# Performance work log

Measured on AMD Instinct MI355X. Metric: run time of the kernel, lower is better.

Reference implementation:

```python
import jax, jax.numpy as jnp
import numpy as np

N, D, H, O, E = 4096, 1024, 4096, 1024, 8
TOP_K = 2

def setup_inputs() -> dict:
    key = jax.random.key(0)
    k = jax.random.split(key, 4)
    x  = jax.random.normal(k[0], (N, D), dtype=jnp.float32)
    Wg = jax.random.normal(k[1], (D, E), dtype=jnp.float32) * (1.0 / np.sqrt(D))
    W1 = jax.random.normal(k[2], (E, D, H), dtype=jnp.float32) * (1.0 / np.sqrt(D))
    b1 = jnp.zeros((E, H), dtype=jnp.float32)
    W2 = jax.random.normal(k[3], (E, H, O), dtype=jnp.float32) * (1.0 / np.sqrt(H))
    b2 = jnp.zeros((E, O), dtype=jnp.float32)
    return {"x": x, "Wg": Wg, "W1": W1, "b1": b1, "W2": W2, "b2": b2}

def reference(x, Wg, W1, b1, W2, b2):
    # Gate: Linear(bias=False) -> ReLU (lin() appends act) -> softmax
    logits = jax.nn.relu(x @ Wg)                      # [N, E]
    probs = jax.nn.softmax(logits, axis=1)            # [N, E]
    top_p, sel = jax.lax.top_k(probs, TOP_K)          # [N, K]
    top_p = top_p / jnp.sum(top_p, axis=-1, keepdims=True)
    # Per-token combine weights over experts: [N, E]
    combine = jnp.sum(jax.nn.one_hot(sel, E, dtype=x.dtype) * top_p[..., None], axis=1)
    # Experts: ReLU(x W1 + b1) -> ReLU(h W2 + b2); final ReLU because lin() adds act on output layer
    h = jax.nn.relu(jnp.einsum('nd,edh->enh', x, W1) + b1[:, None, :])   # [E, N, H]
    y = jax.nn.relu(jnp.einsum('enh,eho->eno', h, W2) + b2[:, None, :])  # [E, N, O]
    out = jnp.einsum('eno,ne->no', y, combine)                            # [N, O]
    return out
```

## Files before the change

### kernel.cpp

```cpp
#include <hip/hip_runtime.h>
#include <cstdint>

#define NTOK 4096
#define DDIM 1024
#define HDIM 4096
#define ODIM 1024
#define NEXP 8
#define NSLOT (2*NTOK)
#define MAXT128 72
#define MAXT256 40

typedef __bf16 bf16x8 __attribute__((ext_vector_type(8)));
typedef float  f32x4  __attribute__((ext_vector_type(4)));
typedef unsigned short ushort8v __attribute__((ext_vector_type(8)));

__device__ __forceinline__ unsigned short f2bf(float f) {
    union { float f; unsigned int u; } v; v.f = f;
    unsigned int r = (v.u + 0x7FFF + ((v.u >> 16) & 1)) >> 16;
    return (unsigned short)r;
}

typedef const void __attribute__((address_space(1)))* gas_ptr;
typedef void       __attribute__((address_space(3)))* las_ptr;

__global__ void gate_kernel(const float* __restrict__ x, const float* __restrict__ Wg,
                            int2* __restrict__ sel, float2* __restrict__ wts,
                            int* __restrict__ counts, unsigned short* __restrict__ xb) {
    int wave = threadIdx.x >> 6;
    int lane = threadIdx.x & 63;
    int n = blockIdx.x * 4 + wave;
    float acc[NEXP];
#pragma unroll
    for (int e = 0; e < NEXP; e++) acc[e] = 0.f;
    const float* xr = x + (size_t)n * DDIM;
    unsigned short* xbr = xb + (size_t)n * DDIM;
#pragma unroll
    for (int i = 0; i < 4; i++) {
        int d = i * 256 + lane * 4;
        float4 xv = *(const float4*)&xr[d];
        ushort4 o;
        o.x = f2bf(xv.x); o.y = f2bf(xv.y); o.z = f2bf(xv.z); o.w = f2bf(xv.w);
        *(ushort4*)&xbr[d] = o;
        const float* wr = Wg + (size_t)d * NEXP;
#pragma unroll
        for (int jj = 0; jj < 4; jj++) {
            float xs = (jj == 0) ? xv.x : (jj == 1) ? xv.y : (jj == 2) ? xv.z : xv.w;
#pragma unroll
            for (int e = 0; e < NEXP; e++)
                acc[e] = fmaf(xs, wr[jj * NEXP + e], acc[e]);
        }
    }
#pragma unroll
    for (int e = 0; e < NEXP; e++) {
#pragma unroll
        for (int off = 32; off >= 1; off >>= 1)
            acc[e] += __shfl_xor(acc[e], off, 64);
    }
    if (lane == 0) {
        float l0 = -1e30f, l1 = -1e30f; int e0 = 0, e1 = 0;
#pragma unroll
        for (int e = 0; e < NEXP; e++) {
            float v = fmaxf(acc[e], 0.f);
            if (v > l0)      { l1 = l0; e1 = e0; l0 = v; e0 = e; }
            else if (v > l1) { l1 = v;  e1 = e; }
        }
        float w0 = 1.f / (1.f + expf(l1 - l0));
        sel[n] = make_int2(e0, e1);
        wts[n] = make_float2(w0, 1.f - w0);
        atomicAdd(&counts[e0], 1);
        atomicAdd(&counts[e1], 1);
    }
}

__global__ void route_kernel(const int2* __restrict__ sel, const float2* __restrict__ wts,
                             const int* __restrict__ counts, int* __restrict__ offsets,
                             int4* __restrict__ t128, int* __restrict__ nt128,
                             int4* __restrict__ t256, int* __restrict__ nt256,
                             int* __restrict__ slot_token, float* __restrict__ slot_weight) {
    __shared__ int cur[NEXP];
    int t = threadIdx.x;
    if (t == 0) {
        int s = 0, n1 = 0, n2 = 0;
        for (int e = 0; e < NEXP; e++) {
            offsets[e] = s; cur[e] = s;
            int c = counts[e];
            for (int r = 0; r < c; r += 128)
                t128[n1++] = make_int4(e, s + r, min(128, c - r), 0);
            for (int r = 0; r < c; r += 256)
                t256[n2++] = make_int4(e, s + r, min(256, c - r), 0);
            s += c;
        }
        offsets[NEXP] = s;
        *nt128 = n1; *nt256 = n2;
    }
    __syncthreads();
    for (int n = t; n < NTOK; n += blockDim.x) {
        int2 se = sel[n]; float2 w = wts[n];
        int p0 = atomicAdd(&cur[se.x], 1);
        slot_token[p0] = n; slot_weight[p0] = w.x;
        int p1 = atomicAdd(&cur[se.y], 1);
        slot_token[p1] = n; slot_weight[p1] = w.y;
    }
}

__global__ void transpose_cast_kernel(const float* __restrict__ src, unsigned short* __restrict__ dst,
                                      int R, int C) {
    __shared__ float tile[64][65];
    int e = blockIdx.z;
    const float* s = src + (size_t)e * R * C;
    unsigned short* d = dst + (size_t)e * R * C;
    int t = threadIdx.x;
    int r0 = blockIdx.y * 64, c0 = blockIdx.x * 64;
#pragma unroll
    for (int p = 0; p < 4; p++) {
        int r = p * 16 + (t >> 4);
        int c = (t & 15) * 4;
        float4 v = *(const float4*)&s[(size_t)(r0 + r) * C + (c0 + c)];
        tile[r][c] = v.x; tile[r][c + 1] = v.y; tile[r][c + 2] = v.z; tile[r][c + 3] = v.w;
    }
    __syncthreads();
    int c = t >> 2, rb = (t & 3) * 16;
#pragma unroll
    for (int j = 0; j < 2; j++) {
        ushort8v v;
#pragma unroll
        for (int i = 0; i < 8; i++) v[i] = f2bf(tile[rb + j * 8 + i][c]);
        *(ushort8v*)&d[(size_t)(c0 + c) * R + (r0 + rb + j * 8)] = v;
    }
}

template <int MODE, int KDIM, int NDIM, int TM, int TN, int WMv>
__global__ __launch_bounds__(256, 2) void moe_gemm_kernel(
    const unsigned short* __restrict__ A,
    const unsigned short* __restrict__ B,
    const float* __restrict__ bias,
    const int4* __restrict__ tile_meta,
    const int* __restrict__ ntiles,
    const int* __restrict__ slot_token,
    const float* __restrict__ slot_weight,
    unsigned short* __restrict__ h,
    float* __restrict__ out) {

    int tileIdx, colBase;
    if constexpr (MODE == 1) {
        tileIdx = blockIdx.y;
        colBase = blockIdx.x * TN;
    } else {
        int j = blockIdx.y;
        tileIdx = blockIdx.x + 8 * (j >> 3);
        colBase = (j & 7) * TN;
    }
    if (tileIdx >= *ntiles) return;
    int4 tm = tile_meta[tileIdx];
    int e = tm.x, slotBase = tm.y, rows = tm.z;

    constexpr int RA = TM / 4, IA = RA / 16;
    constexpr int RB = TN / 4, IB = RB / 16;
    constexpr int NI = KDIM / 32;

    __shared__ __align__(16) unsigned short As[2][TM * 32];
    __shared__ __align__(16) unsigned short Bs[2][TN * 32];

    int tid = threadIdx.x;
    int w = tid >> 6, l = tid & 63;
    int quad = l >> 4, lr = l & 15;
    int wm = w % WMv, wn = w / WMv;

    int rl = l >> 2;
    int g = (l & 3) ^ ((l >> 3) & 3);

    const unsigned short* ag[IA];
    const unsigned short* bg[IB];
    const unsigned short* Be = B + (size_t)e * NDIM * KDIM;
#pragma unroll
    for (int j = 0; j < IA; j++) {
        int r = w * RA + j * 16 + rl;
        int slot = min(slotBase + r, NSLOT - 1);
        if constexpr (MODE == 1) {
            int tok = slot_token[slot];
            ag[j] = A + (size_t)tok * KDIM + g * 8;
        } else {
            ag[j] = A + (size_t)slot * KDIM + g * 8;
        }
    }
#pragma unroll
    for (int j = 0; j < IB; j++) {
        int r = w * RB + j * 16 + rl;
        bg[j] = Be + (size_t)(colBase + r) * KDIM + g * 8;
    }

    f32x4 zero = {0.f, 0.f, 0.f, 0.f};
    f32x4 acc[8][4];
#pragma unroll
    for (int m = 0; m < 8; m++)
#pragma unroll
        for (int n = 0; n < 4; n++) acc[m][n] = zero;

    int su = (quad ^ ((lr >> 1) & 3)) * 16;

    auto issue = [&](int k, int s) {
        unsigned short* AsW = &As[s][w * RA * 32];
        unsigned short* BsW = &Bs[s][w * RB * 32];
#pragma unroll
        for (int j = 0; j < IA; j++)
            __builtin_amdgcn_global_load_lds((gas_ptr)(ag[j] + k * 32), (las_ptr)(AsW + j * 512), 16, 0, 0);
#pragma unroll
        for (int j = 0; j < IB; j++)
            __builtin_amdgcn_global_load_lds((gas_ptr)(bg[j] + k * 32), (las_ptr)(BsW + j * 512), 16, 0, 0);
    };
    auto compute = [&](int s) {
        const char* A_ = (const char*)As[s];
        const char* B_ = (const char*)Bs[s];
        bf16x8 af[8], bf[4];
#pragma unroll
        for (int m = 0; m < 8; m++)
            af[m] = *(const bf16x8*)(A_ + (wm * 128 + m * 16 + lr) * 64 + su);
#pragma unroll
        for (int n = 0; n < 4; n++)
            bf[n] = *(const bf16x8*)(B_ + (wn * 64 + n * 16 + lr) * 64 + su);
#pragma unroll
        for (int m = 0; m < 8; m++)
#pragma unroll
            for (int n = 0; n < 4; n++)
                acc[m][n] = __builtin_amdgcn_mfma_f32_16x16x32_bf16(af[m], bf[n], acc[m][n], 0, 0, 0);
    };

    issue(0, 0);
    for (int k = 0; k < NI - 1; k++) {
        issue(k + 1, (k + 1) & 1);
        asm volatile("s_waitcnt vmcnt(6)" ::: "memory");
        asm volatile("s_barrier" ::: "memory");
        compute(k & 1);
        asm volatile("s_barrier" ::: "memory");
    }
    asm volatile("s_waitcnt vmcnt(0)" ::: "memory");
    asm volatile("s_barrier" ::: "memory");
    compute((NI - 1) & 1);

    if constexpr (MODE == 1) {
        const float* bv = bias + e * NDIM;
#pragma unroll
        for (int n = 0; n < 4; n++) {
            int gc = colBase + wn * 64 + n * 16 + lr;
            float b = bv[gc];
#pragma unroll
            for (int m = 0; m < 8; m++) {
                int rloc = wm * 128 + m * 16 + quad * 4;
#pragma unroll
                for (int i = 0; i < 4; i++) {
                    int r = rloc + i;
                    if (r < rows) {
                        float v = fmaxf(acc[m][n][i] + b, 0.f);
                        h[(size_t)(slotBase + r) * NDIM + gc] = f2bf(v);
                    }
                }
            }
        }
    } else {
        const float* bv = bias + e * NDIM;
#pragma unroll
        for (int m = 0; m < 8; m++) {
            int rloc = wm * 128 + m * 16 + quad * 4;
#pragma unroll
            for (int i = 0; i < 4; i++) {
                int r = rloc + i;
                if (r >= rows) continue;
                int s = slotBase + r;
                int tok = slot_token[s];
                float wgt = slot_weight[s];
                float* orow = out + (size_t)tok * ODIM;
#pragma unroll
                for (int n = 0; n < 4; n++) {
                    int gc = colBase + wn * 64 + n * 16 + lr;
                    float v = fmaxf(acc[m][n][i] + bv[gc], 0.f) * wgt;
                    atomicAdd(&orow[gc], v);
                }
            }
        }
    }
}

extern "C" void kernel_launch(void* const* d_in, const int* in_sizes, int n_in,
                              void* d_out, int out_size, void* d_ws, size_t ws_size,
                              hipStream_t stream) {
    const float* x  = (const float*)d_in[0];
    const float* Wg = (const float*)d_in[1];
    const float* W1 = (const float*)d_in[2];
    const float* b1 = (const float*)d_in[3];
    const float* W2 = (const float*)d_in[4];
    const float* b2 = (const float*)d_in[5];
    float* out = (float*)d_out;

    char* ws = (char*)d_ws;
    int*    counts      = (int*)(ws + 0);
    int*    offsets     = (int*)(ws + 64);
    int*    nt128       = (int*)(ws + 128);
    int*    nt256       = (int*)(ws + 132);
    int4*   t128        = (int4*)(ws + 256);
    int4*   t256        = (int4*)(ws + 2048);
    int2*   sel         = (int2*)(ws + 4096);
    float2* wts         = (float2*)(ws + 36864);
    int*    slot_token  = (int*)(ws + 69632);
    float*  slot_weight = (float*)(ws + 102400);
    unsigned short* xb  = (unsigned short*)(ws + 2097152);
    unsigned short* W1T = (unsigned short*)(ws + 10485760);
    unsigned short* W2T = (unsigned short*)(ws + 77594624);
    unsigned short* hbf = (unsigned short*)(ws + 144703488);

    hipMemsetAsync(d_out, 0, (size_t)NTOK * ODIM * sizeof(float), stream);
    hipMemsetAsync(ws, 0, 256, stream);

    gate_kernel<<<NTOK / 4, 256, 0, stream>>>(x, Wg, sel, wts, counts, xb);
    route_kernel<<<1, 512, 0, stream>>>(sel, wts, counts, offsets, t128, nt128, t256, nt256,
                                        slot_token, slot_weight);

    transpose_cast_kernel<<<dim3(HDIM / 64, DDIM / 64, NEXP), 256, 0, stream>>>(W1, W1T, DDIM, HDIM);
    transpose_cast_kernel<<<dim3(ODIM / 64, HDIM / 64, NEXP), 256, 0, stream>>>(W2, W2T, HDIM, ODIM);

    moe_gemm_kernel<1, DDIM, HDIM, 128, 256, 1><<<dim3(HDIM / 256, MAXT128), 256, 0, stream>>>(
        xb, W1T, b1, t128, nt128, slot_token, slot_weight, hbf, nullptr);
    moe_gemm_kernel<2, HDIM, ODIM, 256, 128, 2><<<dim3(8, MAXT256), 256, 0, stream>>>(
        hbf, W2T, b2, t256, nt256, slot_token, slot_weight, nullptr, out);
}
```

Before: 773.5 us.

## Replace MoE GEMMs with 8-wave 256x256 tile kernel with staged K=64 pipeline

Both expert GEMMs now use a single 512-thread kernel with 256x256 output tiles and a K step of 64. Global-to-LDS loads are split into four half-tiles that are interleaved with four MFMA phases, with s_setprio raised around the MFMA blocks. LDS uses an XOR swizzle over 8 slots. The larger tile raises arithmetic intensity and improves overlap of loads with compute. In exchange it uses 128KB of LDS and issues many barriers per K step, and the first GEMM now runs on 256-row tiles, which adds padding waste for experts with few tokens.

Measured after the change: 774.2 us. No clear change (+0.1%).

```diff
diff --git a/kernel.cpp b/kernel.cpp
--- a/kernel.cpp
+++ b/kernel.cpp
@@ -129,8 +129,8 @@
     }
 }
 
-template <int MODE, int KDIM, int NDIM, int TM, int TN, int WMv>
-__global__ __launch_bounds__(256, 2) void moe_gemm_kernel(
+template <int MODE, int KDIM, int NDIM>
+__global__ __launch_bounds__(512, 2) void moe_gemm8_kernel(
     const unsigned short* __restrict__ A,
     const unsigned short* __restrict__ B,
     const float* __restrict__ bias,
@@ -141,53 +141,58 @@
     unsigned short* __restrict__ h,
     float* __restrict__ out) {
 
-    int tileIdx, colBase;
-    if constexpr (MODE == 1) {
-        tileIdx = blockIdx.y;
-        colBase = blockIdx.x * TN;
-    } else {
-        int j = blockIdx.y;
-        tileIdx = blockIdx.x + 8 * (j >> 3);
-        colBase = (j & 7) * TN;
-    }
+    int tileIdx = blockIdx.y;
+    int colBase = blockIdx.x * 256;
     if (tileIdx >= *ntiles) return;
     int4 tm = tile_meta[tileIdx];
     int e = tm.x, slotBase = tm.y, rows = tm.z;
 
-    constexpr int RA = TM / 4, IA = RA / 16;
-    constexpr int RB = TN / 4, IB = RB / 16;
-    constexpr int NI = KDIM / 32;
-
-    __shared__ __align__(16) unsigned short As[2][TM * 32];
-    __shared__ __align__(16) unsigned short Bs[2][TN * 32];
+    constexpr int NT = KDIM / 64;
+
+    __shared__ __align__(16) unsigned short As[2][16384];
+    __shared__ __align__(16) unsigned short Bs[2][16384];
 
     int tid = threadIdx.x;
-    int w = tid >> 6, l = tid & 63;
-    int quad = l >> 4, lr = l & 15;
-    int wm = w % WMv, wn = w / WMv;
-
-    int rl = l >> 2;
-    int g = (l & 3) ^ ((l >> 3) & 3);
-
-    const unsigned short* ag[IA];
-    const unsigned short* bg[IB];
+    int w = tid >> 6, lane = tid & 63;
+    int quad = lane >> 4, lr = lane & 15;
+    int wm = w >> 2, wn = w & 3;
+
     const unsigned short* Be = B + (size_t)e * NDIM * KDIM;
-#pragma unroll
-    for (int j = 0; j < IA; j++) {
-        int r = w * RA + j * 16 + rl;
+
+    int g = (lane & 7) ^ ((lane >> 3) & 7);
+    unsigned int aoff[4], boff[4];
+#pragma unroll
+    for (int i = 0; i < 4; i++) {
+        int hh = i >> 1, c = i & 1;
+        int r = hh * 128 + c * 64 + w * 8 + (lane >> 3);
         int slot = min(slotBase + r, NSLOT - 1);
-        if constexpr (MODE == 1) {
-            int tok = slot_token[slot];
-            ag[j] = A + (size_t)tok * KDIM + g * 8;
-        } else {
-            ag[j] = A + (size_t)slot * KDIM + g * 8;
-        }
-    }
-#pragma unroll
-    for (int j = 0; j < IB; j++) {
-        int r = w * RB + j * 16 + rl;
-        bg[j] = Be + (size_t)(colBase + r) * KDIM + g * 8;
-    }
+        if constexpr (MODE == 1) aoff[i] = (unsigned)(slot_token[slot] * KDIM + g * 8);
+        else                     aoff[i] = (unsigned)(slot * KDIM + g * 8);
+        boff[i] = (unsigned)((colBase + r) * KDIM + g * 8);
+    }
+
+    auto stage = [&](int t, int sb, int half, bool isA) {
+        const unsigned short* base = isA ? A : Be;
+        const unsigned int* off = isA ? aoff : boff;
+        char* lb = (char*)(isA ? &As[sb][0] : &Bs[sb][0]) + half * 16384;
+#pragma unroll
+        for (int c = 0; c < 2; c++) {
+            __builtin_amdgcn_global_load_lds(
+                (gas_ptr)(base + off[half * 2 + c] + t * 64),
+                (las_ptr)(lb + (c * 512 + w * 64) * 16), 16, 0, 0);
+        }
+    };
+
+    auto ldA = [&](int b, int rbase, int kk) -> bf16x8 {
+        int row = rbase + lr;
+        int sl = (kk * 4 + quad) ^ (row & 7);
+        return *(const bf16x8*)((const char*)&As[0][0] + b * 32768 + row * 128 + sl * 16);
+    };
+    auto ldB = [&](int b, int rbase, int kk) -> bf16x8 {
+        int row = rbase + lr;
+        int sl = (kk * 4 + quad) ^ (row & 7);
+        return *(const bf16x8*)((const char*)&Bs[0][0] + b * 32768 + row * 128 + sl * 16);
+    };
 
     f32x4 zero = {0.f, 0.f, 0.f, 0.f};
     f32x4 acc[8][4];
@@ -196,61 +201,111 @@
 #pragma unroll
         for (int n = 0; n < 4; n++) acc[m][n] = zero;
 
-    int su = (quad ^ ((lr >> 1) & 3)) * 16;
-
-    auto issue = [&](int k, int s) {
-        unsigned short* AsW = &As[s][w * RA * 32];
-        unsigned short* BsW = &Bs[s][w * RB * 32];
-#pragma unroll
-        for (int j = 0; j < IA; j++)
-            __builtin_amdgcn_global_load_lds((gas_ptr)(ag[j] + k * 32), (las_ptr)(AsW + j * 512), 16, 0, 0);
-#pragma unroll
-        for (int j = 0; j < IB; j++)
-            __builtin_amdgcn_global_load_lds((gas_ptr)(bg[j] + k * 32), (las_ptr)(BsW + j * 512), 16, 0, 0);
-    };
-    auto compute = [&](int s) {
-        const char* A_ = (const char*)As[s];
-        const char* B_ = (const char*)Bs[s];
-        bf16x8 af[8], bf[4];
-#pragma unroll
-        for (int m = 0; m < 8; m++)
-            af[m] = *(const bf16x8*)(A_ + (wm * 128 + m * 16 + lr) * 64 + su);
-#pragma unroll
-        for (int n = 0; n < 4; n++)
-            bf[n] = *(const bf16x8*)(B_ + (wn * 64 + n * 16 + lr) * 64 + su);
-#pragma unroll
-        for (int m = 0; m < 8; m++)
-#pragma unroll
-            for (int n = 0; n < 4; n++)
-                acc[m][n] = __builtin_amdgcn_mfma_f32_16x16x32_bf16(af[m], bf[n], acc[m][n], 0, 0, 0);
-    };
-
-    issue(0, 0);
-    for (int k = 0; k < NI - 1; k++) {
-        issue(k + 1, (k + 1) & 1);
-        asm volatile("s_waitcnt vmcnt(6)" ::: "memory");
-        asm volatile("s_barrier" ::: "memory");
-        compute(k & 1);
-        asm volatile("s_barrier" ::: "memory");
-    }
-    asm volatile("s_waitcnt vmcnt(0)" ::: "memory");
-    asm volatile("s_barrier" ::: "memory");
-    compute((NI - 1) & 1);
+    stage(0, 0, 0, true);  stage(0, 0, 1, true);
+    stage(0, 0, 0, false); stage(0, 0, 1, false);
+
+    for (int t = 0; t < NT; ++t) {
+        const int b = t & 1, sb = b ^ 1;
+        const bool st = (t + 1 < NT);
+        const int ts = t + 1;
+        bf16x8 afr[4][2], bf0[2][2], bf1[2][2];
+
+        if (st) stage(ts, sb, 0, true);
+        if (st) asm volatile("s_waitcnt vmcnt(2)" ::: "memory");
+        else    asm volatile("s_waitcnt vmcnt(0)" ::: "memory");
+        __builtin_amdgcn_s_barrier();
+#pragma unroll
+        for (int mi = 0; mi < 4; mi++)
+#pragma unroll
+            for (int kk = 0; kk < 2; kk++)
+                afr[mi][kk] = ldA(b, wm * 128 + mi * 16, kk);
+#pragma unroll
+        for (int ni = 0; ni < 2; ni++)
+#pragma unroll
+            for (int kk = 0; kk < 2; kk++)
+                bf0[ni][kk] = ldB(b, wn * 64 + ni * 16, kk);
+        asm volatile("s_waitcnt lgkmcnt(0)" ::: "memory");
+        __builtin_amdgcn_s_setprio(1);
+#pragma unroll
+        for (int mi = 0; mi < 4; mi++)
+#pragma unroll
+            for (int ni = 0; ni < 2; ni++)
+#pragma unroll
+                for (int kk = 0; kk < 2; kk++)
+                    acc[mi][ni] = __builtin_amdgcn_mfma_f32_16x16x32_bf16(
+                        afr[mi][kk], bf0[ni][kk], acc[mi][ni], 0, 0, 0);
+        __builtin_amdgcn_s_setprio(0);
+        __builtin_amdgcn_s_barrier();
+
+#pragma unroll
+        for (int ni = 0; ni < 2; ni++)
+#pragma unroll
+            for (int kk = 0; kk < 2; kk++)
+                bf1[ni][kk] = ldB(b, wn * 64 + 32 + ni * 16, kk);
+        if (st) stage(ts, sb, 1, true);
+        __builtin_amdgcn_s_barrier();
+        asm volatile("s_waitcnt lgkmcnt(0)" ::: "memory");
+        __builtin_amdgcn_s_setprio(1);
+#pragma unroll
+        for (int mi = 0; mi < 4; mi++)
+#pragma unroll
+            for (int ni = 0; ni < 2; ni++)
+#pragma unroll
+                for (int kk = 0; kk < 2; kk++)
+                    acc[mi][2 + ni] = __builtin_amdgcn_mfma_f32_16x16x32_bf16(
+                        afr[mi][kk], bf1[ni][kk], acc[mi][2 + ni], 0, 0, 0);
+        __builtin_amdgcn_s_setprio(0);
+        __builtin_amdgcn_s_barrier();
+
+#pragma unroll
+        for (int mi = 0; mi < 4; mi++)
+#pragma unroll
+            for (int kk = 0; kk < 2; kk++)
+                afr[mi][kk] = ldA(b, wm * 128 + 64 + mi * 16, kk);
+        if (st) stage(ts, sb, 0, false);
+        __builtin_amdgcn_s_barrier();
+        asm volatile("s_waitcnt lgkmcnt(0)" ::: "memory");
+        __builtin_amdgcn_s_setprio(1);
+#pragma unroll
+        for (int mi = 0; mi < 4; mi++)
+#pragma unroll
+            for (int ni = 0; ni < 2; ni++)
+#pragma unroll
+                for (int kk = 0; kk < 2; kk++)
+                    acc[4 + mi][ni] = __builtin_amdgcn_mfma_f32_16x16x32_bf16(
+                        afr[mi][kk], bf0[ni][kk], acc[4 + mi][ni], 0, 0, 0);
+        __builtin_amdgcn_s_setprio(0);
+        __builtin_amdgcn_s_barrier();
+
+        if (st) stage(ts, sb, 1, false);
+        __builtin_amdgcn_s_barrier();
+        __builtin_amdgcn_s_setprio(1);
+#pragma unroll
+        for (int mi = 0; mi < 4; mi++)
+#pragma unroll
+            for (int ni = 0; ni < 2; ni++)
+#pragma unroll
+                for (int kk = 0; kk < 2; kk++)
+                    acc[4 + mi][2 + ni] = __builtin_amdgcn_mfma_f32_16x16x32_bf16(
+                        afr[mi][kk], bf1[ni][kk], acc[4 + mi][2 + ni], 0, 0, 0);
+        __builtin_amdgcn_s_setprio(0);
+        __builtin_amdgcn_s_barrier();
+    }
 
     if constexpr (MODE == 1) {
         const float* bv = bias + e * NDIM;
 #pragma unroll
         for (int n = 0; n < 4; n++) {
             int gc = colBase + wn * 64 + n * 16 + lr;
-            float b = bv[gc];
+            float bb = bv[gc];
 #pragma unroll
             for (int m = 0; m < 8; m++) {
-                int rloc = wm * 128 + m * 16 + quad * 4;
+                int rl = wm * 128 + m * 16 + quad * 4;
 #pragma unroll
                 for (int i = 0; i < 4; i++) {
-                    int r = rloc + i;
+                    int r = rl + i;
                     if (r < rows) {
-                        float v = fmaxf(acc[m][n][i] + b, 0.f);
+                        float v = fmaxf(acc[m][n][i] + bb, 0.f);
                         h[(size_t)(slotBase + r) * NDIM + gc] = f2bf(v);
                     }
                 }
@@ -260,10 +315,10 @@
         const float* bv = bias + e * NDIM;
 #pragma unroll
         for (int m = 0; m < 8; m++) {
-            int rloc = wm * 128 + m * 16 + quad * 4;
+            int rl = wm * 128 + m * 16 + quad * 4;
 #pragma unroll
             for (int i = 0; i < 4; i++) {
-                int r = rloc + i;
+                int r = rl + i;
                 if (r >= rows) continue;
                 int s = slotBase + r;
                 int tok = slot_token[s];
@@ -317,8 +372,8 @@
     transpose_cast_kernel<<<dim3(HDIM / 64, DDIM / 64, NEXP), 256, 0, stream>>>(W1, W1T, DDIM, HDIM);
     transpose_cast_kernel<<<dim3(ODIM / 64, HDIM / 64, NEXP), 256, 0, stream>>>(W2, W2T, HDIM, ODIM);
 
-    moe_gemm_kernel<1, DDIM, HDIM, 128, 256, 1><<<dim3(HDIM / 256, MAXT128), 256, 0, stream>>>(
-        xb, W1T, b1, t128, nt128, slot_token, slot_weight, hbf, nullptr);
-    moe_gemm_kernel<2, HDIM, ODIM, 256, 128, 2><<<dim3(8, MAXT256), 256, 0, stream>>>(
+    moe_gemm8_kernel<1, DDIM, HDIM><<<dim3(HDIM / 256, MAXT256), 512, 0, stream>>>(
+        xb, W1T, b1, t256, nt256, slot_token, slot_weight, hbf, nullptr);
+    moe_gemm8_kernel<2, HDIM, ODIM><<<dim3(ODIM / 256, MAXT256), 512, 0, stream>>>(
         hbf, W2T, b2, t256, nt256, slot_token, slot_weight, nullptr, out);
 }
```

## Rework MoE GEMM with triple-buffered LDS pipeline, tile remapping, 128-row second GEMM

Applied to the files above, without the earlier changes.

Both expert GEMMs move to a single templated kernel with a three-stage LDS ring buffer. Loads are issued two k-steps ahead, and fragments are read into registers before a barrier, followed by the MFMA block at raised wave priority. Workgroup IDs are remapped so that groups of 8 tiles share a column across consecutive blocks, which is meant to improve L2 reuse. The second GEMM now uses 128-row tiles with 128-wide columns and an occupancy hint of 3, so more blocks run at once but more atomics are issued per output. This adds LDS pressure and relies on hand-counted vmcnt values.

New measurement: 723.5 us. 1.07x faster.

```diff
diff --git a/kernel.cpp b/kernel.cpp
--- a/kernel.cpp
+++ b/kernel.cpp
@@ -129,8 +129,8 @@
     }
 }
 
-template <int MODE, int KDIM, int NDIM, int TM, int TN, int WMv>
-__global__ __launch_bounds__(256, 2) void moe_gemm_kernel(
+template <int MODE, int KDIM, int NDIM, int TN, int WN, int MINW, int NCOL>
+__global__ __launch_bounds__(256, MINW) void moe_gemm_kernel(
     const unsigned short* __restrict__ A,
     const unsigned short* __restrict__ B,
     const float* __restrict__ bias,
@@ -141,116 +141,127 @@
     unsigned short* __restrict__ h,
     float* __restrict__ out) {
 
-    int tileIdx, colBase;
-    if constexpr (MODE == 1) {
-        tileIdx = blockIdx.y;
-        colBase = blockIdx.x * TN;
-    } else {
-        int j = blockIdx.y;
-        tileIdx = blockIdx.x + 8 * (j >> 3);
-        colBase = (j & 7) * TN;
-    }
-    if (tileIdx >= *ntiles) return;
-    int4 tm = tile_meta[tileIdx];
+    constexpr int WM = 4 / WN;
+    constexpr int FM = 128 / WM / 16;
+    constexpr int FN = TN / WN / 16;
+    constexpr int NT = KDIM / 32;
+    constexpr int LB = TN / 64;
+
+    constexpr int nwg = NCOL * MAXT128;
+    int bid = blockIdx.y * NCOL + blockIdx.x;
+    int o = (bid & 7) * (nwg >> 3) + (bid >> 3);
+    int tg = o / (8 * NCOL);
+    int rem = o - tg * (8 * NCOL);
+    int col = rem >> 3;
+    int tile = tg * 8 + (rem & 7);
+    if (tile >= *ntiles) return;
+    int colBase = col * TN;
+
+    int4 tm = tile_meta[tile];
     int e = tm.x, slotBase = tm.y, rows = tm.z;
 
-    constexpr int RA = TM / 4, IA = RA / 16;
-    constexpr int RB = TN / 4, IB = RB / 16;
-    constexpr int NI = KDIM / 32;
-
-    __shared__ __align__(16) unsigned short As[2][TM * 32];
-    __shared__ __align__(16) unsigned short Bs[2][TN * 32];
+    __shared__ __align__(16) unsigned short As[3][128 * 32];
+    __shared__ __align__(16) unsigned short Bs[3][TN * 32];
 
     int tid = threadIdx.x;
-    int w = tid >> 6, l = tid & 63;
-    int quad = l >> 4, lr = l & 15;
-    int wm = w % WMv, wn = w / WMv;
-
-    int rl = l >> 2;
-    int g = (l & 3) ^ ((l >> 3) & 3);
-
-    const unsigned short* ag[IA];
-    const unsigned short* bg[IB];
+    int w = tid >> 6, lane = tid & 63;
+    int quad = lane >> 4, lr = lane & 15;
+    int wm = w / WN, wn = w % WN;
+
     const unsigned short* Be = B + (size_t)e * NDIM * KDIM;
-#pragma unroll
-    for (int j = 0; j < IA; j++) {
-        int r = w * RA + j * 16 + rl;
+
+    int srow = tid >> 2;
+    int g = (tid & 3) ^ ((tid >> 3) & 3);
+    unsigned int aoff[2];
+    unsigned int boff[LB];
+#pragma unroll
+    for (int i = 0; i < 2; i++) {
+        int r = srow + i * 64;
         int slot = min(slotBase + r, NSLOT - 1);
-        if constexpr (MODE == 1) {
-            int tok = slot_token[slot];
-            ag[j] = A + (size_t)tok * KDIM + g * 8;
+        if constexpr (MODE == 1) aoff[i] = (unsigned)(slot_token[slot] * KDIM + g * 8);
+        else                     aoff[i] = (unsigned)(slot * KDIM + g * 8);
+    }
+#pragma unroll
+    for (int i = 0; i < LB; i++)
+        boff[i] = (unsigned)((colBase + srow + i * 64) * KDIM + g * 8);
+
+    auto stage = [&](int t, int sbuf) {
+        char* Ab = (char*)&As[sbuf][0] + (size_t)(w * 64) * 16;
+        char* Bb = (char*)&Bs[sbuf][0] + (size_t)(w * 64) * 16;
+#pragma unroll
+        for (int i = 0; i < 2; i++)
+            __builtin_amdgcn_global_load_lds((gas_ptr)(A + aoff[i] + t * 32),
+                                             (las_ptr)(Ab + i * 4096), 16, 0, 0);
+#pragma unroll
+        for (int i = 0; i < LB; i++)
+            __builtin_amdgcn_global_load_lds((gas_ptr)(Be + boff[i] + t * 32),
+                                             (las_ptr)(Bb + i * 4096), 16, 0, 0);
+    };
+
+    auto ldfrag = [&](const unsigned short* base, int R) -> bf16x8 {
+        int s = quad ^ ((R >> 1) & 3);
+        return *(const bf16x8*)((const char*)base + R * 64 + s * 16);
+    };
+
+    f32x4 zero = {0.f, 0.f, 0.f, 0.f};
+    f32x4 acc[FM][FN];
+#pragma unroll
+    for (int m = 0; m < FM; m++)
+#pragma unroll
+        for (int n = 0; n < FN; n++) acc[m][n] = zero;
+
+    stage(0, 0);
+    stage(1, 1);
+    int sb = 2, rb = 0;
+    for (int t = 0; t < NT; ++t) {
+        if (t + 2 < NT) {
+            stage(t + 2, sb);
+            if constexpr (LB == 4) asm volatile("s_waitcnt vmcnt(12)" ::: "memory");
+            else                   asm volatile("s_waitcnt vmcnt(8)" ::: "memory");
+        } else if (t + 1 < NT) {
+            if constexpr (LB == 4) asm volatile("s_waitcnt vmcnt(6)" ::: "memory");
+            else                   asm volatile("s_waitcnt vmcnt(4)" ::: "memory");
         } else {
-            ag[j] = A + (size_t)slot * KDIM + g * 8;
-        }
-    }
-#pragma unroll
-    for (int j = 0; j < IB; j++) {
-        int r = w * RB + j * 16 + rl;
-        bg[j] = Be + (size_t)(colBase + r) * KDIM + g * 8;
-    }
-
-    f32x4 zero = {0.f, 0.f, 0.f, 0.f};
-    f32x4 acc[8][4];
-#pragma unroll
-    for (int m = 0; m < 8; m++)
-#pragma unroll
-        for (int n = 0; n < 4; n++) acc[m][n] = zero;
-
-    int su = (quad ^ ((lr >> 1) & 3)) * 16;
-
-    auto issue = [&](int k, int s) {
-        unsigned short* AsW = &As[s][w * RA * 32];
-        unsigned short* BsW = &Bs[s][w * RB * 32];
-#pragma unroll
-        for (int j = 0; j < IA; j++)
-            __builtin_amdgcn_global_load_lds((gas_ptr)(ag[j] + k * 32), (las_ptr)(AsW + j * 512), 16, 0, 0);
-#pragma unroll
-        for (int j = 0; j < IB; j++)
-            __builtin_amdgcn_global_load_lds((gas_ptr)(bg[j] + k * 32), (las_ptr)(BsW + j * 512), 16, 0, 0);
-    };
-    auto compute = [&](int s) {
-        const char* A_ = (const char*)As[s];
-        const char* B_ = (const char*)Bs[s];
-        bf16x8 af[8], bf[4];
-#pragma unroll
-        for (int m = 0; m < 8; m++)
-            af[m] = *(const bf16x8*)(A_ + (wm * 128 + m * 16 + lr) * 64 + su);
-#pragma unroll
-        for (int n = 0; n < 4; n++)
-            bf[n] = *(const bf16x8*)(B_ + (wn * 64 + n * 16 + lr) * 64 + su);
-#pragma unroll
-        for (int m = 0; m < 8; m++)
-#pragma unroll
-            for (int n = 0; n < 4; n++)
+            asm volatile("s_waitcnt vmcnt(0)" ::: "memory");
+        }
+        __builtin_amdgcn_s_barrier();
+
+        bf16x8 af[FM], bf[FN];
+        const unsigned short* Ar = As[rb];
+        const unsigned short* Br = Bs[rb];
+#pragma unroll
+        for (int m = 0; m < FM; m++) af[m] = ldfrag(Ar, wm * (128 / WM) + m * 16 + lr);
+#pragma unroll
+        for (int n = 0; n < FN; n++) bf[n] = ldfrag(Br, wn * (TN / WN) + n * 16 + lr);
+        asm volatile("s_waitcnt lgkmcnt(0)" ::: "memory");
+        __builtin_amdgcn_s_barrier();
+
+        __builtin_amdgcn_s_setprio(1);
+#pragma unroll
+        for (int m = 0; m < FM; m++)
+#pragma unroll
+            for (int n = 0; n < FN; n++)
                 acc[m][n] = __builtin_amdgcn_mfma_f32_16x16x32_bf16(af[m], bf[n], acc[m][n], 0, 0, 0);
-    };
-
-    issue(0, 0);
-    for (int k = 0; k < NI - 1; k++) {
-        issue(k + 1, (k + 1) & 1);
-        asm volatile("s_waitcnt vmcnt(6)" ::: "memory");
-        asm volatile("s_barrier" ::: "memory");
-        compute(k & 1);
-        asm volatile("s_barrier" ::: "memory");
-    }
-    asm volatile("s_waitcnt vmcnt(0)" ::: "memory");
-    asm volatile("s_barrier" ::: "memory");
-    compute((NI - 1) & 1);
+        __builtin_amdgcn_s_setprio(0);
+
+        sb = (sb == 2) ? 0 : sb + 1;
+        rb = (rb == 2) ? 0 : rb + 1;
+    }
 
     if constexpr (MODE == 1) {
         const float* bv = bias + e * NDIM;
 #pragma unroll
-        for (int n = 0; n < 4; n++) {
-            int gc = colBase + wn * 64 + n * 16 + lr;
-            float b = bv[gc];
-#pragma unroll
-            for (int m = 0; m < 8; m++) {
-                int rloc = wm * 128 + m * 16 + quad * 4;
+        for (int n = 0; n < FN; n++) {
+            int gc = colBase + wn * (TN / WN) + n * 16 + lr;
+            float bb = bv[gc];
+#pragma unroll
+            for (int m = 0; m < FM; m++) {
+                int rl = wm * (128 / WM) + m * 16 + quad * 4;
 #pragma unroll
                 for (int i = 0; i < 4; i++) {
-                    int r = rloc + i;
+                    int r = rl + i;
                     if (r < rows) {
-                        float v = fmaxf(acc[m][n][i] + b, 0.f);
+                        float v = fmaxf(acc[m][n][i] + bb, 0.f);
                         h[(size_t)(slotBase + r) * NDIM + gc] = f2bf(v);
                     }
                 }
@@ -259,19 +270,19 @@
     } else {
         const float* bv = bias + e * NDIM;
 #pragma unroll
-        for (int m = 0; m < 8; m++) {
-            int rloc = wm * 128 + m * 16 + quad * 4;
+        for (int m = 0; m < FM; m++) {
+            int rl = wm * (128 / WM) + m * 16 + quad * 4;
 #pragma unroll
             for (int i = 0; i < 4; i++) {
-                int r = rloc + i;
+                int r = rl + i;
                 if (r >= rows) continue;
                 int s = slotBase + r;
                 int tok = slot_token[s];
                 float wgt = slot_weight[s];
                 float* orow = out + (size_t)tok * ODIM;
 #pragma unroll
-                for (int n = 0; n < 4; n++) {
-                    int gc = colBase + wn * 64 + n * 16 + lr;
+                for (int n = 0; n < FN; n++) {
+                    int gc = colBase + wn * (TN / WN) + n * 16 + lr;
                     float v = fmaxf(acc[m][n][i] + bv[gc], 0.f) * wgt;
                     atomicAdd(&orow[gc], v);
                 }
@@ -317,8 +328,8 @@
     transpose_cast_kernel<<<dim3(HDIM / 64, DDIM / 64, NEXP), 256, 0, stream>>>(W1, W1T, DDIM, HDIM);
     transpose_cast_kernel<<<dim3(ODIM / 64, HDIM / 64, NEXP), 256, 0, stream>>>(W2, W2T, HDIM, ODIM);
 
-    moe_gemm_kernel<1, DDIM, HDIM, 128, 256, 1><<<dim3(HDIM / 256, MAXT128), 256, 0, stream>>>(
+    moe_gemm_kernel<1, DDIM, HDIM, 256, 4, 2, 16><<<dim3(16, MAXT128), 256, 0, stream>>>(
         xb, W1T, b1, t128, nt128, slot_token, slot_weight, hbf, nullptr);
-    moe_gemm_kernel<2, HDIM, ODIM, 256, 128, 2><<<dim3(8, MAXT256), 256, 0, stream>>>(
-        hbf, W2T, b2, t256, nt256, slot_token, slot_weight, nullptr, out);
-}
+    moe_gemm_kernel<2, HDIM, ODIM, 128, 2, 3, 8><<<dim3(8, MAXT128), 256, 0, stream>>>(
+        hbf, W2T, b2, t128, nt128, slot_token, slot_weight, nullptr, out);
+}
```
